# Performance work log

Measured on AMD Instinct MI355X. Metric: run time of the kernel, lower is better.

Reference implementation:

```python
import jax, jax.numpy as jnp
import numpy as np

N_X, N_UNITS, N_Y, N_U = 64, 256, 32, 64
BATCH = 32768


def setup_inputs() -> dict:
    key = jax.random.key(0)
    ks = jax.random.split(key, 10)
    nz = 2 * N_X + N_UNITS
    return {
        "u": jax.random.normal(ks[0], (BATCH, N_U, 1), dtype=jnp.float32),
        "x0": jax.random.normal(ks[1], (BATCH, N_X, 1), dtype=jnp.float32),
        # learned parameters (scaled down so H stays well-conditioned and tanh unsaturated)
        "B_2": 0.1 * jax.random.normal(ks[2], (N_X, N_U), dtype=jnp.float32),
        "C_2": 0.1 * jax.random.normal(ks[3], (N_Y, N_X), dtype=jnp.float32),
        "D_12": 0.1 * jax.random.normal(ks[4], (N_UNITS, N_U), dtype=jnp.float32),
        "D_21": 0.1 * jax.random.normal(ks[5], (N_Y, N_UNITS), dtype=jnp.float32),
        "b": 0.1 * jax.random.normal(ks[6], (N_X + N_UNITS + N_Y, 1), dtype=jnp.float32),
        "X": (1.0 / np.sqrt(nz)) * jax.random.normal(ks[7], (nz, nz), dtype=jnp.float32),
        "Y1": 0.1 * jax.random.normal(ks[8], (N_X, N_X), dtype=jnp.float32),
        # fixed IQC multipliers (train_qsr=False): Q nsd, R=I so Rinv=I; S stored transposed
        "S_t": 0.1 * jax.random.normal(ks[9], (N_U, N_Y), dtype=jnp.float32),
        "Q": -jnp.eye(N_Y, dtype=jnp.float32),
        "Rinv": jnp.eye(N_U, dtype=jnp.float32),
    }


def _constrained_weights(B_2, C_2, D_12, D_21, X, S_t, Q, Rinv):
    """Port of REN.updateConstrainedWeights (train_qsr=False). Returns C_1, D_11, lam."""
    n_x, n_units = B_2.shape[0], D_12.shape[0]
    n_y = C_2.shape[0]
    nz = 2 * n_x + n_units
    C2_ = S_t @ C_2                       # [n_u, n_x]
    D21_ = S_t @ D_21 - D_12.T            # [n_u, n_units]
    H = X.T @ X + 1e-3 * jnp.eye(nz, dtype=X.dtype)
    lT1 = jnp.concatenate([C2_.T, D21_.T, B_2], axis=0)          # [nz, n_u]
    H = H + lT1 @ Rinv @ lT1.T
    lT2 = jnp.concatenate([C_2.T, D_21.T, jnp.zeros((n_x, n_y), dtype=X.dtype)], axis=0)
    H = H - lT2 @ Q @ lT2.T
    H_21 = H[n_x:n_x + n_units, :n_x]
    H_22 = H[n_x:n_x + n_units, n_x:n_x + n_units]
    C_1 = -H_21                           # [n_units, n_x]
    lam = 0.5 * jnp.diag(H_22)            # Lambda diagonal, > 0 since H is PD
    # L = tril(-(H_22 - diag(H_22))) == -strictly_lower(H_22)
    D_11 = -jnp.tril(H_22, k=-1)          # strictly lower triangular [n_units, n_units]
    return C_1, D_11, lam


def _forward(u, x0, B_2, C_2, D_12, D_21, b, X, Y1, S_t, Q, Rinv):
    n_x, n_units = B_2.shape[0], D_12.shape[0]
    C_1, D_11, lam = _constrained_weights(B_2, C_2, D_12, D_21, X, S_t, Q, Rinv)
    u2 = u[:, :, 0]                       # [B, n_u]
    x2 = x0[:, :, 0]                      # [B, n_x]
    b_w = b[n_x:n_x + n_units, 0]         # [n_units]
    b_y = b[n_x + n_units:, 0]            # [n_y]
    # precompute the non-recurrent part of the pre-activation for all units
    v = x2 @ C_1.T + u2 @ D_12.T + b_w    # [B, n_units]
    # NOTE: the source uses D_11 row (i_unit - 1), not i_unit (faithful to original code).
    # For i=0 the source uses term2 = 0; D_11 is strictly lower so the full-row dot
    # against the partially-filled w (zeros beyond index i) matches D_11[i-1, :i] @ w[:i].
    Drows = jnp.concatenate([jnp.zeros((1, n_units), dtype=D_11.dtype), D_11[:-1]], axis=0)
    batch = u2.shape[0]

    def step(w, i):
        wi = jnp.tanh((v[:, i] + w @ Drows[i]) / lam[i])   # [B]
        w = w.at[:, i].set(wi)
        return w, None

    w0 = jnp.zeros((batch, n_units), dtype=v.dtype)
    w, _ = jax.lax.scan(step, w0, jnp.arange(n_units))
    y = x2 @ C_2.T + w @ D_21.T + b_y     # [B, n_y]
    return y[:, :, None]                  # [B, n_y, 1]


def reference(u, x0, B_2, C_2, D_12, D_21, b, X, Y1, S_t, Q, Rinv):
    return _forward(u, x0, B_2, C_2, D_12, D_21, b, X, Y1, S_t, Q, Rinv)
```

## Files before the change

kernel.cpp:

```cpp
#include <hip/hip_runtime.h>
#include <hip/hip_bf16.h>

typedef __attribute__((ext_vector_type(8))) short short8;
typedef __attribute__((ext_vector_type(4))) float floatx4;
typedef __attribute__((ext_vector_type(2))) float floatx2;

#define MFMA16 __builtin_amdgcn_mfma_f32_16x16x32_bf16

__device__ inline unsigned short bf16_rn(float f) {
    return (unsigned short)((__float_as_uint(f) + 0x8000u) >> 16);
}
__device__ __attribute__((always_inline)) inline short8 pack8v(float4 a, float4 b) {
    union { short8 s; unsigned int u[4]; } r;
    union { __hip_bfloat162 h; unsigned int u; } c;
    c.h = __float22bfloat162_rn(make_float2(a.x, a.y)); r.u[0] = c.u;
    c.h = __float22bfloat162_rn(make_float2(a.z, a.w)); r.u[1] = c.u;
    c.h = __float22bfloat162_rn(make_float2(b.x, b.y)); r.u[2] = c.u;
    c.h = __float22bfloat162_rn(make_float2(b.z, b.w)); r.u[3] = c.u;
    return r.s;
}

__global__ __launch_bounds__(64) void ren_prep13(
    const float* __restrict__ B2, const float* __restrict__ C2,
    const float* __restrict__ D12, const float* __restrict__ D21,
    const float* __restrict__ St, const float* __restrict__ Q,
    const float* __restrict__ Rinv,
    float* __restrict__ lT1, float* __restrict__ t1,
    float* __restrict__ lT2, float* __restrict__ t2,
    unsigned short* __restrict__ Wvb, unsigned short* __restrict__ C2b,
    unsigned short* __restrict__ D21b)
{
    const int t = threadIdx.x;
    const int blk = blockIdx.x;
    if (blk >= 384) {
        const int id = (blk - 384) * 64 + t;
        if (id < 16384) {
            Wvb[(id >> 6) * 128 + 64 + (id & 63)] = bf16_rn(D12[id]);
        } else if (id < 16384 + 2048) {
            C2b[id - 16384] = bf16_rn(C2[id - 16384]);
        } else if (id < 16384 + 2048 + 8192) {
            D21b[id - 18432] = bf16_rn(D21[id - 18432]);
        }
        return;
    }

    __shared__ float stl[64 * 33];
    __shared__ float colbuf[32];
    __shared__ float s1[64];

    const int r = blk;
    const int c = t;
#pragma unroll
    for (int j = 0; j < 32; j++) {
        const int id = j * 64 + t;
        stl[(id >> 5) * 33 + (id & 31)] = St[id];
    }
    if (t < 32)
        colbuf[t] = (r < 64) ? C2[t * 64 + r]
                  : (r < 320 ? D21[t * 256 + (r - 64)] : 0.f);
    __syncthreads();

    float v1;
    if (r < 64) {
        float s = 0.f;
#pragma unroll
        for (int p = 0; p < 32; p++) s += stl[c * 33 + p] * colbuf[p];
        v1 = s;
    } else if (r < 320) {
        float s = 0.f;
#pragma unroll
        for (int p = 0; p < 32; p++) s += stl[c * 33 + p] * colbuf[p];
        v1 = s - D12[(r - 64) * 64 + c];
    } else {
        v1 = B2[(r - 320) * 64 + c];
    }
    s1[c] = v1;
    lT1[r * 64 + c] = v1;
    if (c < 32) {
        const float v2 = (r < 320) ? colbuf[c] : 0.f;
        lT2[r * 32 + c] = v2;
    }
    __syncthreads();

    float a = 0.f;
#pragma unroll
    for (int k = 0; k < 64; k++) a += s1[k] * Rinv[k * 64 + c];
    t1[r * 64 + c] = a;

    if (c < 32) {
        float bq = 0.f;
#pragma unroll
        for (int k = 0; k < 32; k++) bq += colbuf[k] * Q[k * 32 + c];
        t2[r * 32 + c] = bq;
    }
}

__global__ __launch_bounds__(320) void ren_prep2(
    const float* __restrict__ X,
    const float* __restrict__ lT1, const float* __restrict__ t1,
    const float* __restrict__ lT2, const float* __restrict__ t2,
    unsigned short* __restrict__ Wvb, unsigned short* __restrict__ Drowsb,
    float* __restrict__ Dpair, float* __restrict__ lamg)
{
    __shared__ float xcol[384];
    const int c = threadIdx.x;
    const int i = blockIdx.x;
    for (int t = c; t < 384; t += 320) xcol[t] = X[t * 384 + 64 + i];
    __syncthreads();

    float f0 = 0.f, f1 = 0.f, f2 = 0.f, f3 = 0.f;
    float ac[8], au[8], bc8[8], bu[8];
#pragma unroll
    for (int kk = 0; kk < 8; kk++) { ac[kk] = X[kk * 384 + c]; au[kk] = xcol[kk]; }
    for (int k0 = 0; k0 < 384; k0 += 16) {
#pragma unroll
        for (int kk = 0; kk < 8; kk++) {
            bc8[kk] = X[(k0 + 8 + kk) * 384 + c]; bu[kk] = xcol[k0 + 8 + kk];
        }
        f0 += au[0] * ac[0]; f1 += au[1] * ac[1];
        f2 += au[2] * ac[2]; f3 += au[3] * ac[3];
        f0 += au[4] * ac[4]; f1 += au[5] * ac[5];
        f2 += au[6] * ac[6]; f3 += au[7] * ac[7];
        if (k0 + 16 < 384) {
#pragma unroll
            for (int kk = 0; kk < 8; kk++) {
                ac[kk] = X[(k0 + 16 + kk) * 384 + c]; au[kk] = xcol[k0 + 16 + kk];
            }
        }
        f0 += bu[0] * bc8[0]; f1 += bu[1] * bc8[1];
        f2 += bu[2] * bc8[2]; f3 += bu[3] * bc8[3];
        f0 += bu[4] * bc8[4]; f1 += bu[5] * bc8[5];
        f2 += bu[6] * bc8[6]; f3 += bu[7] * bc8[7];
    }

    const float* __restrict__ t1r = t1 + (64 + i) * 64;
    const float* __restrict__ l1r = lT1 + c * 64;
#pragma unroll
    for (int m4 = 0; m4 < 16; m4++) {
        const float4 lv = *(const float4*)(l1r + m4 * 4);
        f0 += t1r[m4 * 4 + 0] * lv.x; f1 += t1r[m4 * 4 + 1] * lv.y;
        f2 += t1r[m4 * 4 + 2] * lv.z; f3 += t1r[m4 * 4 + 3] * lv.w;
    }
    const float* __restrict__ t2r = t2 + (64 + i) * 32;
    const float* __restrict__ l2r = lT2 + c * 32;
#pragma unroll
    for (int m4 = 0; m4 < 8; m4++) {
        const float4 lv = *(const float4*)(l2r + m4 * 4);
        f0 -= t2r[m4 * 4 + 0] * lv.x; f1 -= t2r[m4 * 4 + 1] * lv.y;
        f2 -= t2r[m4 * 4 + 2] * lv.z; f3 -= t2r[m4 * 4 + 3] * lv.w;
    }
    float acc = (f0 + f1) + (f2 + f3) + (((64 + i) == c) ? 0.001f : 0.f);

    if (c < 64) {
        Wvb[i * 128 + c] = bf16_rn(-acc);
    } else {
        const int cb = c - 64;
        if (cb == i) lamg[i] = 5.7707801635558536f / acc;
        if (i < 255) {
            const float dv = (cb <= i - 1) ? -acc : 0.f;
            Drowsb[(i + 1) * 256 + cb] = bf16_rn(dv);
            const int row = i + 1;
            if ((row >> 4) == (cb >> 4)) {
                const int q = row & 15, p = cb & 15;
                Dpair[(row >> 4) * 256 + (q >> 1) * 32 + p * 2 + (q & 1)] = dv;
            }
        } else {
            Drowsb[cb] = 0;
        }
    }
}

__device__ __attribute__((always_inline)) inline void triangle16(
    float (&vl)[16], float (&wl)[16],
    const float* __restrict__ dblk, const float* __restrict__ lam)
{
#pragma unroll
    for (int tq = 0; tq < 8; tq++) {
        floatx2 a2;
        a2[0] = vl[2 * tq]; a2[1] = vl[2 * tq + 1];
#pragma unroll
        for (int p4 = 0; p4 < tq; p4++) {
            const float4 d4 = *(const float4*)&dblk[tq * 32 + p4 * 4];
            floatx2 de; de[0] = d4.x; de[1] = d4.y;
            floatx2 dz; dz[0] = d4.z; dz[1] = d4.w;
            a2 += de * wl[2 * p4];
            a2 += dz * wl[2 * p4 + 1];
        }
        floatx2 lm2; lm2[0] = lam[2 * tq]; lm2[1] = lam[2 * tq + 1];
        a2 *= lm2;
        const float e0 = __builtin_amdgcn_exp2f(a2[0]);
        const float e1 = __builtin_amdgcn_exp2f(a2[1]);
        wl[2 * tq]     = 1.f - 2.f * __builtin_amdgcn_rcpf(e0 + 1.f);
        wl[2 * tq + 1] = 1.f - 2.f * __builtin_amdgcn_rcpf(e1 + 1.f);
    }
}

__global__ __launch_bounds__(64, 2) void ren_main(
    const float* __restrict__ u, const float* __restrict__ x0,
    const float* __restrict__ b,
    const unsigned short* __restrict__ Wvb,
    const unsigned short* __restrict__ Drowsb,
    const float* __restrict__ Dpair,
    const float* __restrict__ lamg,
    const unsigned short* __restrict__ C2b,
    const unsigned short* __restrict__ D21b,
    float* __restrict__ out)
{
    __shared__ float buf[16][20];
    __shared__ float dblk[256];
    __shared__ float lamsh[256];
    __shared__ float bsh[256];
    __shared__ short8 wsh[8 * 64];

    const int L = threadIdx.x;
    const int col = L & 15;
    const int quad = L >> 4;
    const int row0 = blockIdx.x * 16;

#pragma unroll
    for (int j = 0; j < 4; j++) {
        lamsh[j * 64 + L] = lamg[j * 64 + L];
        bsh[j * 64 + L]   = b[64 + j * 64 + L];
    }
    const short8 zero8 = {0, 0, 0, 0, 0, 0, 0, 0};
#pragma unroll
    for (int c = 0; c < 8; c++) wsh[c * 64 + L] = zero8;

    short8 zf[4];
#pragma unroll
    for (int c = 0; c < 4; c++) {
        const float* p = (c < 2 ? x0 : u) + (long)(row0 + col) * 64 + (c & 1) * 32 + quad * 8;
        const float4 pa = *(const float4*)p;
        const float4 pb = *(const float4*)(p + 4);
        zf[c] = pack8v(pa, pb);
    }

    float4 dcur = *(const float4*)(Dpair + 4 * L);
    floatx4 acc0 = {0.f, 0.f, 0.f, 0.f}, acc1 = {0.f, 0.f, 0.f, 0.f};
    {
        short8 v0 = *(const short8*)(Wvb + col * 128 + quad * 8);
        short8 v1 = *(const short8*)(Wvb + col * 128 + 32 + quad * 8);
        short8 v2 = *(const short8*)(Wvb + col * 128 + 64 + quad * 8);
        short8 v3 = *(const short8*)(Wvb + col * 128 + 96 + quad * 8);
        acc0 = MFMA16(zf[0], v0, acc0, 0, 0, 0);
        acc1 = MFMA16(zf[1], v1, acc1, 0, 0, 0);
        acc0 = MFMA16(zf[2], v2, acc0, 0, 0, 0);
        acc1 = MFMA16(zf[3], v3, acc1, 0, 0, 0);
    }

#pragma unroll 1
    for (int n = 0; n < 15; n++) {
        const int rb = 16 * (n + 1) + col;
        float4 dnxt = *(const float4*)(Dpair + (n + 1) * 256 + 4 * L);
        short8 vf[4];
#pragma unroll
        for (int c = 0; c < 4; c++)
            vf[c] = *(const short8*)(Wvb + rb * 128 + c * 32 + quad * 8);
        short8 hf[8];
#pragma unroll
        for (int c = 0; c < 8; c++)
            hf[c] = *(const short8*)(Drowsb + rb * 256 + c * 32 + quad * 8);

        *(float4*)&dblk[4 * L] = dcur;
        const float bwv = bsh[16 * n + col];
#pragma unroll
        for (int r = 0; r < 4; r++)
            buf[quad * 4 + r][col] = acc0[r] + acc1[r] + bwv;

        float vl[16], wl[16];
#pragma unroll
        for (int p4 = 0; p4 < 4; p4++) {
            const float4 tv = *(const float4*)&buf[col][p4 * 4];
            vl[p4 * 4 + 0] = tv.x; vl[p4 * 4 + 1] = tv.y;
            vl[p4 * 4 + 2] = tv.z; vl[p4 * 4 + 3] = tv.w;
        }

        triangle16(vl, wl, dblk, &lamsh[16 * n]);

        {
            float4 wa, wb;
            if (quad & 1) {
                wa = make_float4(wl[8], wl[9], wl[10], wl[11]);
                wb = make_float4(wl[12], wl[13], wl[14], wl[15]);
            } else {
                wa = make_float4(wl[0], wl[1], wl[2], wl[3]);
                wb = make_float4(wl[4], wl[5], wl[6], wl[7]);
            }
            const short8 nf = pack8v(wa, wb);
            if ((quad >> 1) == (n & 1)) wsh[(n >> 1) * 64 + L] = nf;
        }

        floatx4 a0 = {0.f, 0.f, 0.f, 0.f}, a1 = {0.f, 0.f, 0.f, 0.f};
        a0 = MFMA16(zf[0], vf[0], a0, 0, 0, 0);
        a1 = MFMA16(zf[1], vf[1], a1, 0, 0, 0);
        a0 = MFMA16(zf[2], vf[2], a0, 0, 0, 0);
        a1 = MFMA16(zf[3], vf[3], a1, 0, 0, 0);
#pragma unroll
        for (int c = 0; c < 8; c++) {
            const short8 wfc = wsh[c * 64 + L];
            if (c & 1) a1 = MFMA16(wfc, hf[c], a1, 0, 0, 0);
            else       a0 = MFMA16(wfc, hf[c], a0, 0, 0, 0);
        }
        acc0 = a0; acc1 = a1; dcur = dnxt;
    }

    {
        *(float4*)&dblk[4 * L] = dcur;
        const float bwv = bsh[240 + col];
#pragma unroll
        for (int r = 0; r < 4; r++)
            buf[quad * 4 + r][col] = acc0[r] + acc1[r] + bwv;

        float vl[16], wl[16];
#pragma unroll
        for (int p4 = 0; p4 < 4; p4++) {
            const float4 tv = *(const float4*)&buf[col][p4 * 4];
            vl[p4 * 4 + 0] = tv.x; vl[p4 * 4 + 1] = tv.y;
            vl[p4 * 4 + 2] = tv.z; vl[p4 * 4 + 3] = tv.w;
        }

        triangle16(vl, wl, dblk, &lamsh[240]);

        float4 wa, wb;
        if (quad & 1) {
            wa = make_float4(wl[8], wl[9], wl[10], wl[11]);
            wb = make_float4(wl[12], wl[13], wl[14], wl[15]);
        } else {
            wa = make_float4(wl[0], wl[1], wl[2], wl[3]);
            wb = make_float4(wl[4], wl[5], wl[6], wl[7]);
        }
        const short8 nf = pack8v(wa, wb);
        if (quad >= 2) wsh[7 * 64 + L] = nf;
    }

    floatx4 y0 = {0.f, 0.f, 0.f, 0.f}, y1 = {0.f, 0.f, 0.f, 0.f};
    {
        const short8 yc0 = *(const short8*)(C2b + col * 64 + quad * 8);
        const short8 yc1 = *(const short8*)(C2b + col * 64 + 32 + quad * 8);
        const short8 yc2 = *(const short8*)(C2b + (16 + col) * 64 + quad * 8);
        const short8 yc3 = *(const short8*)(C2b + (16 + col) * 64 + 32 + quad * 8);
        y0 = MFMA16(zf[0], yc0, y0, 0, 0, 0);
        y1 = MFMA16(zf[0], yc2, y1, 0, 0, 0);
        y0 = MFMA16(zf[1], yc1, y0, 0, 0, 0);
        y1 = MFMA16(zf[1], yc3, y1, 0, 0, 0);
    }
#pragma unroll
    for (int c = 0; c < 8; c++) {
        const short8 wfc = wsh[c * 64 + L];
        const short8 b0 = *(const short8*)(D21b + col * 256 + c * 32 + quad * 8);
        const short8 b1 = *(const short8*)(D21b + (16 + col) * 256 + c * 32 + quad * 8);
        y0 = MFMA16(wfc, b0, y0, 0, 0, 0);
        y1 = MFMA16(wfc, b1, y1, 0, 0, 0);
    }
    const float by0 = b[320 + col];
    const float by1 = b[336 + col];
#pragma unroll
    for (int r = 0; r < 4; r++) {
        out[(long)(row0 + quad * 4 + r) * 32 + col]      = y0[r] + by0;
        out[(long)(row0 + quad * 4 + r) * 32 + 16 + col] = y1[r] + by1;
    }
}

extern "C" void kernel_launch(void* const* d_in, const int* in_sizes, int n_in,
                              void* d_out, int out_size, void* d_ws, size_t ws_size,
                              hipStream_t stream)
{
    const float* u    = (const float*)d_in[0];
    const float* x0   = (const float*)d_in[1];
    const float* B2   = (const float*)d_in[2];
    const float* C2   = (const float*)d_in[3];
    const float* D12  = (const float*)d_in[4];
    const float* D21  = (const float*)d_in[5];
    const float* b    = (const float*)d_in[6];
    const float* X    = (const float*)d_in[7];
    const float* St   = (const float*)d_in[9];
    const float* Q    = (const float*)d_in[10];
    const float* Rinv = (const float*)d_in[11];
    float* out = (float*)d_out;

    float* ws     = (float*)d_ws;
    float* lT1    = ws;
    float* t1     = lT1 + 384 * 64;
    float* lT2    = t1 + 384 * 64;
    float* t2     = lT2 + 384 * 32;
    float* lamg   = t2 + 384 * 32;
    float* Dpair  = lamg + 256;
    unsigned short* Drowsb = (unsigned short*)(Dpair + 16 * 256);
    unsigned short* Wvb    = Drowsb + 256 * 256;
    unsigned short* C2b    = Wvb + 256 * 128;
    unsigned short* D21b   = C2b + 32 * 64;

    ren_prep13<<<dim3(800), dim3(64), 0, stream>>>(B2, C2, D12, D21, St, Q, Rinv,
                                                   lT1, t1, lT2, t2, Wvb, C2b, D21b);
    ren_prep2<<<dim3(256), dim3(320), 0, stream>>>(X, lT1, t1, lT2, t2,
                                                   Wvb, Drowsb, Dpair, lamg);

    const int batch = in_sizes[0] / 64;
    ren_main<<<dim3(batch / 16), dim3(64), 0, stream>>>(u, x0, b, Wvb, Drowsb,
                                                        Dpair, lamg, C2b, D21b, out);
}
```

Before: 149.3 us.

## Process two 16-row batch tiles per wavefront to share weights and hide latency

```diff
diff --git a/kernel.cpp b/kernel.cpp
--- a/kernel.cpp
+++ b/kernel.cpp
@@ -170,32 +170,41 @@
     }
 }
 
-__device__ __attribute__((always_inline)) inline void triangle16(
-    float (&vl)[16], float (&wl)[16],
+__device__ __attribute__((always_inline)) inline void triangle16x2(
+    float (&vlA)[16], float (&wlA)[16],
+    float (&vlB)[16], float (&wlB)[16],
     const float* __restrict__ dblk, const float* __restrict__ lam)
 {
 #pragma unroll
     for (int tq = 0; tq < 8; tq++) {
-        floatx2 a2;
-        a2[0] = vl[2 * tq]; a2[1] = vl[2 * tq + 1];
+        floatx2 aA, bA, aB, bB;
+        aA[0] = vlA[2 * tq]; aA[1] = vlA[2 * tq + 1];
+        aB[0] = vlB[2 * tq]; aB[1] = vlB[2 * tq + 1];
+        bA[0] = 0.f; bA[1] = 0.f;
+        bB[0] = 0.f; bB[1] = 0.f;
 #pragma unroll
         for (int p4 = 0; p4 < tq; p4++) {
             const float4 d4 = *(const float4*)&dblk[tq * 32 + p4 * 4];
             floatx2 de; de[0] = d4.x; de[1] = d4.y;
             floatx2 dz; dz[0] = d4.z; dz[1] = d4.w;
-            a2 += de * wl[2 * p4];
-            a2 += dz * wl[2 * p4 + 1];
-        }
+            aA += de * wlA[2 * p4];  bA += dz * wlA[2 * p4 + 1];
+            aB += de * wlB[2 * p4];  bB += dz * wlB[2 * p4 + 1];
+        }
+        aA += bA; aB += bB;
         floatx2 lm2; lm2[0] = lam[2 * tq]; lm2[1] = lam[2 * tq + 1];
-        a2 *= lm2;
-        const float e0 = __builtin_amdgcn_exp2f(a2[0]);
-        const float e1 = __builtin_amdgcn_exp2f(a2[1]);
-        wl[2 * tq]     = 1.f - 2.f * __builtin_amdgcn_rcpf(e0 + 1.f);
-        wl[2 * tq + 1] = 1.f - 2.f * __builtin_amdgcn_rcpf(e1 + 1.f);
-    }
-}
-
-__global__ __launch_bounds__(64, 2) void ren_main(
+        aA *= lm2; aB *= lm2;
+        const float e0A = __builtin_amdgcn_exp2f(aA[0]);
+        const float e1A = __builtin_amdgcn_exp2f(aA[1]);
+        const float e0B = __builtin_amdgcn_exp2f(aB[0]);
+        const float e1B = __builtin_amdgcn_exp2f(aB[1]);
+        wlA[2 * tq]     = 1.f - 2.f * __builtin_amdgcn_rcpf(e0A + 1.f);
+        wlA[2 * tq + 1] = 1.f - 2.f * __builtin_amdgcn_rcpf(e1A + 1.f);
+        wlB[2 * tq]     = 1.f - 2.f * __builtin_amdgcn_rcpf(e0B + 1.f);
+        wlB[2 * tq + 1] = 1.f - 2.f * __builtin_amdgcn_rcpf(e1B + 1.f);
+    }
+}
+
+__global__ __launch_bounds__(64, 1) void ren_main(
     const float* __restrict__ u, const float* __restrict__ x0,
     const float* __restrict__ b,
     const unsigned short* __restrict__ Wvb,
@@ -206,16 +215,18 @@
     const unsigned short* __restrict__ D21b,
     float* __restrict__ out)
 {
-    __shared__ float buf[16][20];
+    __shared__ float bufA[16][20];
+    __shared__ float bufB[16][20];
     __shared__ float dblk[256];
     __shared__ float lamsh[256];
     __shared__ float bsh[256];
-    __shared__ short8 wsh[8 * 64];
+    __shared__ short8 wshA[8 * 64];
+    __shared__ short8 wshB[8 * 64];
 
     const int L = threadIdx.x;
     const int col = L & 15;
     const int quad = L >> 4;
-    const int row0 = blockIdx.x * 16;
+    const int row0 = blockIdx.x * 32;
 
 #pragma unroll
     for (int j = 0; j < 4; j++) {
@@ -224,28 +235,34 @@
     }
     const short8 zero8 = {0, 0, 0, 0, 0, 0, 0, 0};
 #pragma unroll
-    for (int c = 0; c < 8; c++) wsh[c * 64 + L] = zero8;
-
-    short8 zf[4];
+    for (int c = 0; c < 8; c++) { wshA[c * 64 + L] = zero8; wshB[c * 64 + L] = zero8; }
+
+    short8 zfA[4], zfB[4];
 #pragma unroll
     for (int c = 0; c < 4; c++) {
-        const float* p = (c < 2 ? x0 : u) + (long)(row0 + col) * 64 + (c & 1) * 32 + quad * 8;
-        const float4 pa = *(const float4*)p;
-        const float4 pb = *(const float4*)(p + 4);
-        zf[c] = pack8v(pa, pb);
+        const float* base = (c < 2 ? x0 : u);
+        const float* pA = base + (long)(row0 + col) * 64 + (c & 1) * 32 + quad * 8;
+        const float* pB = base + (long)(row0 + 16 + col) * 64 + (c & 1) * 32 + quad * 8;
+        zfA[c] = pack8v(*(const float4*)pA, *(const float4*)(pA + 4));
+        zfB[c] = pack8v(*(const float4*)pB, *(const float4*)(pB + 4));
     }
 
     float4 dcur = *(const float4*)(Dpair + 4 * L);
-    floatx4 acc0 = {0.f, 0.f, 0.f, 0.f}, acc1 = {0.f, 0.f, 0.f, 0.f};
+    floatx4 accA0 = {0.f, 0.f, 0.f, 0.f}, accA1 = {0.f, 0.f, 0.f, 0.f};
+    floatx4 accB0 = {0.f, 0.f, 0.f, 0.f}, accB1 = {0.f, 0.f, 0.f, 0.f};
     {
         short8 v0 = *(const short8*)(Wvb + col * 128 + quad * 8);
         short8 v1 = *(const short8*)(Wvb + col * 128 + 32 + quad * 8);
         short8 v2 = *(const short8*)(Wvb + col * 128 + 64 + quad * 8);
         short8 v3 = *(const short8*)(Wvb + col * 128 + 96 + quad * 8);
-        acc0 = MFMA16(zf[0], v0, acc0, 0, 0, 0);
-        acc1 = MFMA16(zf[1], v1, acc1, 0, 0, 0);
-        acc0 = MFMA16(zf[2], v2, acc0, 0, 0, 0);
-        acc1 = MFMA16(zf[3], v3, acc1, 0, 0, 0);
+        accA0 = MFMA16(zfA[0], v0, accA0, 0, 0, 0);
+        accB0 = MFMA16(zfB[0], v0, accB0, 0, 0, 0);
+        accA1 = MFMA16(zfA[1], v1, accA1, 0, 0, 0);
+        accB1 = MFMA16(zfB[1], v1, accB1, 0, 0, 0);
+        accA0 = MFMA16(zfA[2], v2, accA0, 0, 0, 0);
+        accB0 = MFMA16(zfB[2], v2, accB0, 0, 0, 0);
+        accA1 = MFMA16(zfA[3], v3, accA1, 0, 0, 0);
+        accB1 = MFMA16(zfB[3], v3, accB1, 0, 0, 0);
     }
 
 #pragma unroll 1
@@ -264,100 +281,148 @@
         *(float4*)&dblk[4 * L] = dcur;
         const float bwv = bsh[16 * n + col];
 #pragma unroll
-        for (int r = 0; r < 4; r++)
-            buf[quad * 4 + r][col] = acc0[r] + acc1[r] + bwv;
-
-        float vl[16], wl[16];
+        for (int r = 0; r < 4; r++) {
+            bufA[quad * 4 + r][col] = accA0[r] + accA1[r] + bwv;
+            bufB[quad * 4 + r][col] = accB0[r] + accB1[r] + bwv;
+        }
+
+        float vlA[16], wlA[16], vlB[16], wlB[16];
 #pragma unroll
         for (int p4 = 0; p4 < 4; p4++) {
-            const float4 tv = *(const float4*)&buf[col][p4 * 4];
-            vl[p4 * 4 + 0] = tv.x; vl[p4 * 4 + 1] = tv.y;
-            vl[p4 * 4 + 2] = tv.z; vl[p4 * 4 + 3] = tv.w;
-        }
-
-        triangle16(vl, wl, dblk, &lamsh[16 * n]);
+            const float4 ta = *(const float4*)&bufA[col][p4 * 4];
+            const float4 tb = *(const float4*)&bufB[col][p4 * 4];
+            vlA[p4 * 4 + 0] = ta.x; vlA[p4 * 4 + 1] = ta.y;
+            vlA[p4 * 4 + 2] = ta.z; vlA[p4 * 4 + 3] = ta.w;
+            vlB[p4 * 4 + 0] = tb.x; vlB[p4 * 4 + 1] = tb.y;
+            vlB[p4 * 4 + 2] = tb.z; vlB[p4 * 4 + 3] = tb.w;
+        }
+
+        triangle16x2(vlA, wlA, vlB, wlB, dblk, &lamsh[16 * n]);
 
         {
-            float4 wa, wb;
+            float4 waA, wbA, waB, wbB;
             if (quad & 1) {
-                wa = make_float4(wl[8], wl[9], wl[10], wl[11]);
-                wb = make_float4(wl[12], wl[13], wl[14], wl[15]);
+                waA = make_float4(wlA[8], wlA[9], wlA[10], wlA[11]);
+                wbA = make_float4(wlA[12], wlA[13], wlA[14], wlA[15]);
+                waB = make_float4(wlB[8], wlB[9], wlB[10], wlB[11]);
+                wbB = make_float4(wlB[12], wlB[13], wlB[14], wlB[15]);
             } else {
-                wa = make_float4(wl[0], wl[1], wl[2], wl[3]);
-                wb = make_float4(wl[4], wl[5], wl[6], wl[7]);
+                waA = make_float4(wlA[0], wlA[1], wlA[2], wlA[3]);
+                wbA = make_float4(wlA[4], wlA[5], wlA[6], wlA[7]);
+                waB = make_float4(wlB[0], wlB[1], wlB[2], wlB[3]);
+                wbB = make_float4(wlB[4], wlB[5], wlB[6], wlB[7]);
             }
-            const short8 nf = pack8v(wa, wb);
-            if ((quad >> 1) == (n & 1)) wsh[(n >> 1) * 64 + L] = nf;
-        }
-
-        floatx4 a0 = {0.f, 0.f, 0.f, 0.f}, a1 = {0.f, 0.f, 0.f, 0.f};
-        a0 = MFMA16(zf[0], vf[0], a0, 0, 0, 0);
-        a1 = MFMA16(zf[1], vf[1], a1, 0, 0, 0);
-        a0 = MFMA16(zf[2], vf[2], a0, 0, 0, 0);
-        a1 = MFMA16(zf[3], vf[3], a1, 0, 0, 0);
+            const short8 nfA = pack8v(waA, wbA);
+            const short8 nfB = pack8v(waB, wbB);
+            if ((quad >> 1) == (n & 1)) {
+                wshA[(n >> 1) * 64 + L] = nfA;
+                wshB[(n >> 1) * 64 + L] = nfB;
+            }
+        }
+
+        floatx4 aA0 = {0.f, 0.f, 0.f, 0.f}, aA1 = {0.f, 0.f, 0.f, 0.f};
+        floatx4 aB0 = {0.f, 0.f, 0.f, 0.f}, aB1 = {0.f, 0.f, 0.f, 0.f};
+        aA0 = MFMA16(zfA[0], vf[0], aA0, 0, 0, 0);
+        aB0 = MFMA16(zfB[0], vf[0], aB0, 0, 0, 0);
+        aA1 = MFMA16(zfA[1], vf[1], aA1, 0, 0, 0);
+        aB1 = MFMA16(zfB[1], vf[1], aB1, 0, 0, 0);
+        aA0 = MFMA16(zfA[2], vf[2], aA0, 0, 0, 0);
+        aB0 = MFMA16(zfB[2], vf[2], aB0, 0, 0, 0);
+        aA1 = MFMA16(zfA[3], vf[3], aA1, 0, 0, 0);
+        aB1 = MFMA16(zfB[3], vf[3], aB1, 0, 0, 0);
 #pragma unroll
         for (int c = 0; c < 8; c++) {
-            const short8 wfc = wsh[c * 64 + L];
-            if (c & 1) a1 = MFMA16(wfc, hf[c], a1, 0, 0, 0);
-            else       a0 = MFMA16(wfc, hf[c], a0, 0, 0, 0);
-        }
-        acc0 = a0; acc1 = a1; dcur = dnxt;
+            const short8 wA = wshA[c * 64 + L];
+            const short8 wB = wshB[c * 64 + L];
+            if (c & 1) {
+                aA1 = MFMA16(wA, hf[c], aA1, 0, 0, 0);
+                aB1 = MFMA16(wB, hf[c], aB1, 0, 0, 0);
+            } else {
+                aA0 = MFMA16(wA, hf[c], aA0, 0, 0, 0);
+                aB0 = MFMA16(wB, hf[c], aB0, 0, 0, 0);
+            }
+        }
+        accA0 = aA0; accA1 = aA1; accB0 = aB0; accB1 = aB1;
+        dcur = dnxt;
     }
 
     {
         *(float4*)&dblk[4 * L] = dcur;
         const float bwv = bsh[240 + col];
 #pragma unroll
-        for (int r = 0; r < 4; r++)
-            buf[quad * 4 + r][col] = acc0[r] + acc1[r] + bwv;
-
-        float vl[16], wl[16];
+        for (int r = 0; r < 4; r++) {
+            bufA[quad * 4 + r][col] = accA0[r] + accA1[r] + bwv;
+            bufB[quad * 4 + r][col] = accB0[r] + accB1[r] + bwv;
+        }
+
+        float vlA[16], wlA[16], vlB[16], wlB[16];
 #pragma unroll
         for (int p4 = 0; p4 < 4; p4++) {
-            const float4 tv = *(const float4*)&buf[col][p4 * 4];
-            vl[p4 * 4 + 0] = tv.x; vl[p4 * 4 + 1] = tv.y;
-            vl[p4 * 4 + 2] = tv.z; vl[p4 * 4 + 3] = tv.w;
-        }
-
-        triangle16(vl, wl, dblk, &lamsh[240]);
-
-        float4 wa, wb;
+            const float4 ta = *(const float4*)&bufA[col][p4 * 4];
+            const float4 tb = *(const float4*)&bufB[col][p4 * 4];
+            vlA[p4 * 4 + 0] = ta.x; vlA[p4 * 4 + 1] = ta.y;
+            vlA[p4 * 4 + 2] = ta.z; vlA[p4 * 4 + 3] = ta.w;
+            vlB[p4 * 4 + 0] = tb.x; vlB[p4 * 4 + 1] = tb.y;
+            vlB[p4 * 4 + 2] = tb.z; vlB[p4 * 4 + 3] = tb.w;
+        }
+
+        triangle16x2(vlA, wlA, vlB, wlB, dblk, &lamsh[240]);
+
+        float4 waA, wbA, waB, wbB;
         if (quad & 1) {
-            wa = make_float4(wl[8], wl[9], wl[10], wl[11]);
-            wb = make_float4(wl[12], wl[13], wl[14], wl[15]);
+            waA = make_float4(wlA[8], wlA[9], wlA[10], wlA[11]);
+            wbA = make_float4(wlA[12], wlA[13], wlA[14], wlA[15]);
+            waB = make_float4(wlB[8], wlB[9], wlB[10], wlB[11]);
+            wbB = make_float4(wlB[12], wlB[13], wlB[14], wlB[15]);
         } else {
-            wa = make_float4(wl[0], wl[1], wl[2], wl[3]);
-            wb = make_float4(wl[4], wl[5], wl[6], wl[7]);
-        }
-        const short8 nf = pack8v(wa, wb);
-        if (quad >= 2) wsh[7 * 64 + L] = nf;
-    }
-
-    floatx4 y0 = {0.f, 0.f, 0.f, 0.f}, y1 = {0.f, 0.f, 0.f, 0.f};
+            waA = make_float4(wlA[0], wlA[1], wlA[2], wlA[3]);
+            wbA = make_float4(wlA[4], wlA[5], wlA[6], wlA[7]);
+            waB = make_float4(wlB[0], wlB[1], wlB[2], wlB[3]);
+            wbB = make_float4(wlB[4], wlB[5], wlB[6], wlB[7]);
+        }
+        const short8 nfA = pack8v(waA, wbA);
+        const short8 nfB = pack8v(waB, wbB);
+        if (quad >= 2) {
+            wshA[7 * 64 + L] = nfA;
+            wshB[7 * 64 + L] = nfB;
+        }
+    }
+
+    floatx4 yA0 = {0.f, 0.f, 0.f, 0.f}, yA1 = {0.f, 0.f, 0.f, 0.f};
+    floatx4 yB0 = {0.f, 0.f, 0.f, 0.f}, yB1 = {0.f, 0.f, 0.f, 0.f};
     {
         const short8 yc0 = *(const short8*)(C2b + col * 64 + quad * 8);
         const short8 yc1 = *(const short8*)(C2b + col * 64 + 32 + quad * 8);
         const short8 yc2 = *(const short8*)(C2b + (16 + col) * 64 + quad * 8);
         const short8 yc3 = *(const short8*)(C2b + (16 + col) * 64 + 32 + quad * 8);
-        y0 = MFMA16(zf[0], yc0, y0, 0, 0, 0);
-        y1 = MFMA16(zf[0], yc2, y1, 0, 0, 0);
-        y0 = MFMA16(zf[1], yc1, y0, 0, 0, 0);
-        y1 = MFMA16(zf[1], yc3, y1, 0, 0, 0);
+        yA0 = MFMA16(zfA[0], yc0, yA0, 0, 0, 0);
+        yB0 = MFMA16(zfB[0], yc0, yB0, 0, 0, 0);
+        yA1 = MFMA16(zfA[0], yc2, yA1, 0, 0, 0);
+        yB1 = MFMA16(zfB[0], yc2, yB1, 0, 0, 0);
+        yA0 = MFMA16(zfA[1], yc1, yA0, 0, 0, 0);
+        yB0 = MFMA16(zfB[1], yc1, yB0, 0, 0, 0);
+        yA1 = MFMA16(zfA[1], yc3, yA1, 0, 0, 0);
+        yB1 = MFMA16(zfB[1], yc3, yB1, 0, 0, 0);
     }
 #pragma unroll
     for (int c = 0; c < 8; c++) {
-        const short8 wfc = wsh[c * 64 + L];
+        const short8 wA = wshA[c * 64 + L];
+        const short8 wB = wshB[c * 64 + L];
         const short8 b0 = *(const short8*)(D21b + col * 256 + c * 32 + quad * 8);
         const short8 b1 = *(const short8*)(D21b + (16 + col) * 256 + c * 32 + quad * 8);
-        y0 = MFMA16(wfc, b0, y0, 0, 0, 0);
-        y1 = MFMA16(wfc, b1, y1, 0, 0, 0);
+        yA0 = MFMA16(wA, b0, yA0, 0, 0, 0);
+        yB0 = MFMA16(wB, b0, yB0, 0, 0, 0);
+        yA1 = MFMA16(wA, b1, yA1, 0, 0, 0);
+        yB1 = MFMA16(wB, b1, yB1, 0, 0, 0);
     }
     const float by0 = b[320 + col];
     const float by1 = b[336 + col];
 #pragma unroll
     for (int r = 0; r < 4; r++) {
-        out[(long)(row0 + quad * 4 + r) * 32 + col]      = y0[r] + by0;
-        out[(long)(row0 + quad * 4 + r) * 32 + 16 + col] = y1[r] + by1;
+        out[(long)(row0 + quad * 4 + r) * 32 + col]           = yA0[r] + by0;
+        out[(long)(row0 + quad * 4 + r) * 32 + 16 + col]      = yA1[r] + by1;
+        out[(long)(row0 + 16 + quad * 4 + r) * 32 + col]      = yB0[r] + by0;
+        out[(long)(row0 + 16 + quad * 4 + r) * 32 + 16 + col] = yB1[r] + by1;
     }
 }
 
@@ -396,6 +461,6 @@
                                                    Wvb, Drowsb, Dpair, lamg);
 
     const int batch = in_sizes[0] / 64;
-    ren_main<<<dim3(batch / 16), dim3(64), 0, stream>>>(u, x0, b, Wvb, Drowsb,
+    ren_main<<<dim3(batch / 32), dim3(64), 0, stream>>>(u, x0, b, Wvb, Drowsb,
                                                         Dpair, lamg, C2b, D21b, out);
 }
```

Measured after the change: 126.9 us. 1.18x faster.
